# Performance work log

Hardware: AMD Instinct MI355X
Metric: run time of the kernel (lower is better)

The kernel has to match this reference:

```python
import jax, jax.numpy as jnp
from jax import lax
import numpy as np

G, K = 8, 9  # deformable groups, 3x3 kernel taps


def conv1x1_bn_relu(x, W, scale, bias):
    # Conv2d 1x1 (no bias) + folded eval-mode BatchNorm (per-channel scale/bias) + ReLU
    y = jnp.einsum('bchw,oc->bohw', x, W)
    return jax.nn.relu(y * scale[None, :, None, None] + bias[None, :, None, None])


def dcn_v2(feat, offset_feat, W_om, b_om, W_dcn, b_dcn):
    # Modulated deformable conv v2, 3x3, stride 1, pad 1, dilation 1,
    # deformable_groups=G, extra_offset_mask: offsets/mask predicted from offset_feat.
    B, C, H, W_ = feat.shape
    Cg = C // G
    om = lax.conv_general_dilated(offset_feat, W_om, (1, 1), ((1, 1), (1, 1)))
    om = om + b_om[None, :, None, None]              # [B, 3*G*K, H, W]
    o1, o2, m = jnp.split(om, 3, axis=1)
    off_y = o1.reshape(B, G, K, H, W_)
    off_x = o2.reshape(B, G, K, H, W_)
    mask = jax.nn.sigmoid(m).reshape(B, G, K, H, W_)
    dk = jnp.arange(3) - 1
    dkh = jnp.repeat(dk, 3)   # tap row offset,  k = kh*3 + kw
    dkw = jnp.tile(dk, 3)     # tap col offset
    hh = jnp.arange(H, dtype=feat.dtype)
    ww = jnp.arange(W_, dtype=feat.dtype)
    py = hh[None, None, None, :, None] + dkh[None, None, :, None, None].astype(feat.dtype) + off_y
    px = ww[None, None, None, None, :] + dkw[None, None, :, None, None].astype(feat.dtype) + off_x
    y0 = jnp.floor(py); x0 = jnp.floor(px)
    ty = py - y0; tx = px - x0
    xg = feat.reshape(B, G, Cg, H * W_)

    def gather(idx):  # idx [B,G,K,H,W] int32 -> [B,G,Cg,K,H,W]
        f = lambda xf, i: xf[:, i]
        return jax.vmap(jax.vmap(f))(xg, idx)

    val = jnp.zeros((B, G, Cg, K, H, W_), dtype=feat.dtype)
    y0i = y0.astype(jnp.int32); x0i = x0.astype(jnp.int32)
    for dy, wy in ((0, 1.0 - ty), (1, ty)):
        iy = y0i + dy
        vy = (iy >= 0) & (iy < H)
        iyc = jnp.clip(iy, 0, H - 1)
        for dx, wx in ((0, 1.0 - tx), (1, tx)):
            ix = x0i + dx
            v = vy & (ix >= 0) & (ix < W_)
            idx = iyc * W_ + jnp.clip(ix, 0, W_ - 1)
            w = (wy * wx) * v.astype(feat.dtype)      # zero-padding outside
            val = val + w[:, :, None] * gather(idx)
    val = val * mask[:, :, None]                      # modulation
    Wd = W_dcn.reshape(W_dcn.shape[0], G, Cg, K)      # [Cout, G, Cg, K]
    out = jnp.einsum('bgckhw,ogck->bohw', val, Wd) + b_dcn[None, :, None, None]
    return out


def setup_inputs() -> dict:
    key = jax.random.key(0)
    ks = jax.random.split(key, 16)
    B, C, H, W_ = 8, 128, 64, 64
    Cd = C // 2  # dcn out channels = 64
    d = {}
    d['feat_l'] = jax.random.normal(ks[0], (B, C, H, W_), jnp.float32)
    d['feat_s'] = jax.random.normal(ks[1], (B, C, H // 2, W_ // 2), jnp.float32)
    d['W_fsm'] = jax.random.normal(ks[2], (C, C), jnp.float32) / np.sqrt(C)
    d['s_fsm'] = 1.0 + 0.1 * jax.random.normal(ks[3], (C,), jnp.float32)
    d['b_fsm'] = 0.1 * jax.random.normal(ks[4], (C,), jnp.float32)
    d['W_off'] = jax.random.normal(ks[5], (C, 2 * C), jnp.float32) / np.sqrt(2 * C)
    d['s_off'] = 1.0 + 0.1 * jax.random.normal(ks[6], (C,), jnp.float32)
    d['b_off'] = 0.1 * jax.random.normal(ks[7], (C,), jnp.float32)
    d['W_om'] = 0.05 * jax.random.normal(ks[8], (3 * G * K, C, 3, 3), jnp.float32)
    d['b_om'] = jnp.zeros((3 * G * K,), jnp.float32)
    d['W_dcn'] = jax.random.normal(ks[9], (Cd, C, 3, 3), jnp.float32) / np.sqrt(C * 9)
    d['b_dcn'] = 0.1 * jax.random.normal(ks[10], (Cd,), jnp.float32)
    d['W_cat'] = jax.random.normal(ks[11], (C, Cd), jnp.float32) / np.sqrt(Cd)
    d['s_cat'] = 1.0 + 0.1 * jax.random.normal(ks[12], (C,), jnp.float32)
    d['b_cat'] = 0.1 * jax.random.normal(ks[13], (C,), jnp.float32)
    return d


def reference(feat_l, feat_s, W_fsm, s_fsm, b_fsm, W_off, s_off, b_off,
              W_om, b_om, W_dcn, b_dcn, W_cat, s_cat, b_cat):
    # nearest upsample x2 (F.interpolate nearest to feat_l spatial size)
    feat_up = jnp.repeat(jnp.repeat(feat_s, 2, axis=2), 2, axis=3)
    feat_arm = conv1x1_bn_relu(feat_l, W_fsm, s_fsm, b_fsm)
    offset = conv1x1_bn_relu(jnp.concatenate([feat_arm, feat_up * 2.0], axis=1),
                             W_off, s_off, b_off)
    feat_align = jax.nn.relu(dcn_v2(feat_up, offset, W_om, b_om, W_dcn, b_dcn))
    feat = conv1x1_bn_relu(feat_align, W_cat, s_cat, b_cat) + feat_arm
    return (feat, feat_arm)
```

## Files before the change

### kernel.cpp

```cpp
#include <hip/hip_runtime.h>


typedef __attribute__((ext_vector_type(8))) short short8;
typedef __attribute__((ext_vector_type(4))) float f32x4;
typedef _Float16 __attribute__((ext_vector_type(2))) h2;

static __device__ __forceinline__ unsigned short f2bf(float x) {
    union { float f; unsigned int u; } v; v.f = x;
    return (unsigned short)((v.u + 0x7FFF + ((v.u >> 16) & 1)) >> 16);
}
static __device__ __forceinline__ unsigned short f2h(float x) {
    union { _Float16 h; unsigned short u; } v; v.h = (_Float16)x;
    return v.u;
}

__global__ __launch_bounds__(256) void k_prep(const float* __restrict__ fs,
        uint4* __restrict__ fsT4, uint4* __restrict__ fsC4,
        const float* __restrict__ W_fsm, const float* __restrict__ W_off,
        const float* __restrict__ W_cat, const float* __restrict__ W_dcn,
        const float* __restrict__ W_om,
        unsigned short* __restrict__ wbfsm, unsigned short* __restrict__ wboff,
        unsigned short* __restrict__ wbcat, unsigned short* __restrict__ wbdcn,
        unsigned short* __restrict__ wb2) {
    __shared__ unsigned short st[64 * 136];
    const int t = threadIdx.x;
    if (blockIdx.x < 128) {
        unsigned int* st32 = (unsigned int*)st;
        const int b = blockIdx.x >> 4;
        const int p0 = (blockIdx.x & 15) << 6;
        for (int i = t; i < 64 * 64; i += 256) {
            int c2 = i >> 6, px = i & 63;
            float v0 = fs[(((b << 7) + 2 * c2) << 10) + p0 + px];
            float v1 = fs[(((b << 7) + 2 * c2 + 1) << 10) + p0 + px];
            st32[px * 68 + c2] = (unsigned int)f2bf(v0) | ((unsigned int)f2bf(v1) << 16);
        }
        __syncthreads();
        for (int i = t; i < 64 * 16; i += 256) {
            int px = i >> 4, q = i & 15;
            fsT4[(((b << 10) + p0 + px) << 4) + q] = ((const uint4*)(st + px * 136))[q];
        }
        __syncthreads();
        for (int i = t; i < 64 * 64; i += 256) {
            int c2 = i >> 6, px = i & 63;
            float v0 = fs[(((b << 7) + 2 * c2) << 10) + p0 + px];
            float v1 = fs[(((b << 7) + 2 * c2 + 1) << 10) + p0 + px];
            st32[px * 68 + c2] = (unsigned int)f2h(v0) | ((unsigned int)f2h(v1) << 16);
        }
        __syncthreads();
        for (int i = t; i < 64 * 16; i += 256) {
            int ci = i >> 6, px = i & 63;
            fsC4[(b << 14) + (ci << 10) + p0 + px] = ((const uint4*)(st + px * 136))[ci];
        }
        return;
    }
    int idx = (blockIdx.x - 128) * 256 + t;
    int lane = idx & 63;
    int ml = lane & 15, kl = (lane >> 4) * 8;
    unsigned short tmp[8];
    if (idx < 2048) {
        int r = idx >> 6;
        int o = (r % 8) * 16 + ml, k0 = (r / 8) * 32 + kl;
#pragma unroll
        for (int j = 0; j < 8; j++) tmp[j] = f2bf(W_fsm[o * 128 + k0 + j]);
        ((uint4*)wbfsm)[idx] = *(const uint4*)tmp;
    } else if (idx < 6144) {
        int i2 = idx - 2048;
        int r = i2 >> 6;
        int o = (r % 8) * 16 + ml, k0 = (r / 8) * 32 + kl;
#pragma unroll
        for (int j = 0; j < 8; j++) {
            int k = k0 + j;
            float f = W_off[o * 256 + k];
            if (k >= 128) f *= 2.0f;
            tmp[j] = f2bf(f);
        }
        ((uint4*)wboff)[i2] = *(const uint4*)tmp;
    } else if (idx < 7168) {
        int i2 = idx - 6144;
        int r = i2 >> 6;
        int o = (r % 8) * 16 + ml, k0 = (r / 8) * 32 + kl;
#pragma unroll
        for (int j = 0; j < 8; j++) tmp[j] = f2bf(W_cat[o * 64 + k0 + j]);
        ((uint4*)wbcat)[i2] = *(const uint4*)tmp;
    } else if (idx < 16384) {
        int i2 = idx - 7168;
        int r = i2 >> 6;
        int o = (r & 3) * 16 + ml, k0 = (r >> 2) * 32 + kl;
#pragma unroll
        for (int j = 0; j < 8; j++) {
            int k = k0 + j;
            int g = k / 144;
            int rem = k - g * 144;
            tmp[j] = f2h(W_dcn[(o * 128 + g * 16 + (rem & 15)) * 9 + (rem >> 4)]);
        }
        ((uint4*)wbdcn)[i2] = *(const uint4*)tmp;
    } else if (idx < 53248) {
        int i2 = idx - 16384;
        int r = i2 >> 6;
        int nt = r & 15, kk = r >> 4;
        int tap = kk >> 2, cc = kk & 3;
        int o = nt * 16 + ml;
        int c0 = cc * 32 + kl;
#pragma unroll
        for (int j = 0; j < 8; j++) {
            float v = (o < 216) ? W_om[(o * 128 + (c0 + j)) * 9 + tap] : 0.0f;
            tmp[j] = f2bf(v);
        }
        ((uint4*)wb2)[i2] = *(const uint4*)tmp;
    }
}

__global__ __launch_bounds__(512, 6) void k12(const float* __restrict__ feat_l,
        const uint4* __restrict__ fsT4,
        const unsigned short* __restrict__ wbf, const unsigned short* __restrict__ wbo,
        const float* __restrict__ s_fsm, const float* __restrict__ b_fsm,
        const float* __restrict__ s_off, const float* __restrict__ b_off,
        float* __restrict__ feat_arm, unsigned short* __restrict__ offT) {
    __shared__ unsigned short A1[64 * 136];
    __shared__ unsigned short A2[64 * 264];
    const int t = threadIdx.x;
    const int b = blockIdx.x >> 6;
    const int h = blockIdx.x & 63;
    const int hw0 = h << 6;
    unsigned int* A1w = (unsigned int*)A1;
    for (int i = t; i < 64 * 64; i += 512) {
        int c2 = i >> 6, px = i & 63;
        float v0 = feat_l[(((b << 7) + 2 * c2) << 12) + hw0 + px];
        float v1 = feat_l[(((b << 7) + 2 * c2 + 1) << 12) + hw0 + px];
        A1w[px * 68 + c2] = (unsigned int)f2bf(v0) | ((unsigned int)f2bf(v1) << 16);
    }
    {
        const int h2 = h >> 1;
        int px2 = t >> 4, q = t & 15;
        uint4 v = fsT4[(((b << 10) + (h2 << 5) + px2) << 4) + q];
        ((uint4*)(A2 + (2 * px2) * 264 + 128))[q] = v;
        ((uint4*)(A2 + (2 * px2 + 1) * 264 + 128))[q] = v;
    }
    __syncthreads();
    const int lane = t & 63;
    const int w = __builtin_amdgcn_readfirstlane(t >> 6);
    const int pq = w & 3;
    const int nh = w >> 2;
    const int m = lane & 15, ko = lane >> 4;
    f32x4 acc[4];
#pragma unroll
    for (int nt2 = 0; nt2 < 4; nt2++) acc[nt2] = (f32x4){0.f, 0.f, 0.f, 0.f};
#pragma unroll
    for (int kk = 0; kk < 4; kk++) {
        short8 av = *(const short8*)(A1 + (pq * 16 + m) * 136 + kk * 32 + ko * 8);
        const uint4* wb = (const uint4*)wbf + (kk * 8 + nh * 4) * 64 + lane;
#pragma unroll
        for (int nt2 = 0; nt2 < 4; nt2++) {
            uint4 bu = wb[nt2 * 64];
            acc[nt2] = __builtin_amdgcn_mfma_f32_16x16x32_bf16(av, *(short8*)&bu, acc[nt2], 0, 0, 0);
        }
    }
    {
        const int px0 = pq * 16 + (ko << 2);
#pragma unroll
        for (int nt2 = 0; nt2 < 4; nt2++) {
            int o = ((nh << 2) + nt2) * 16 + m;
            float sc = s_fsm[o], bi = b_fsm[o];
            f32x4 v;
#pragma unroll
            for (int r = 0; r < 4; r++) {
                float vv = fmaf(acc[nt2][r], sc, bi);
                vv = vv > 0.f ? vv : 0.f;
                v[r] = vv;
                A2[(px0 + r) * 264 + o] = f2bf(vv);
            }
            *(f32x4*)(feat_arm + ((((b << 7) + o) << 12) + hw0 + px0)) = v;
        }
    }
    __syncthreads();
    f32x4 acc2[4];
#pragma unroll
    for (int nt2 = 0; nt2 < 4; nt2++) acc2[nt2] = (f32x4){0.f, 0.f, 0.f, 0.f};
#pragma unroll
    for (int kk = 0; kk < 8; kk++) {
        short8 av = *(const short8*)(A2 + (pq * 16 + m) * 264 + kk * 32 + ko * 8);
        const uint4* wb = (const uint4*)wbo + (kk * 8 + nh * 4) * 64 + lane;
#pragma unroll
        for (int nt2 = 0; nt2 < 4; nt2++) {
            uint4 bu = wb[nt2 * 64];
            acc2[nt2] = __builtin_amdgcn_mfma_f32_16x16x32_bf16(av, *(short8*)&bu, acc2[nt2], 0, 0, 0);
        }
    }
    __syncthreads();
#pragma unroll
    for (int nt2 = 0; nt2 < 4; nt2++) {
        int o = ((nh << 2) + nt2) * 16 + m;
        float sc = s_off[o], bi = b_off[o];
#pragma unroll
        for (int r = 0; r < 4; r++) {
            float v = fmaf(acc2[nt2][r], sc, bi);
            v = v > 0.f ? v : 0.f;
            A2[(pq * 16 + ko * 4 + r) * 264 + o] = f2bf(v);
        }
    }
    __syncthreads();
    for (int i = t; i < 64 * 16; i += 512) {
        int px = i >> 4, q = i & 15;
        ((uint4*)offT)[(((b << 12) + hw0 + px) << 4) + q] = ((const uint4*)(A2 + px * 264))[q];
    }
}

static __device__ __forceinline__ void dcn_prep(int kk, int ko, const float* omrow,
        float fh, float fw, const uint4* __restrict__ fsC4, int b14,
        uint4& c00, uint4& c01, uint4& c10, uint4& c11,
        float& w00, float& w01, float& w10, float& w11) {
    int k0 = (kk << 5) + (ko << 3);
    int g = k0 / 144;
    int rem = k0 - g * 144;
    int tap = rem >> 4;
    int c0 = rem & 15;
    int ch = g * 9 + tap;
    float oy = omrow[ch];
    float ox = omrow[72 + ch];
    float mmv = omrow[144 + ch];
    mmv = 1.0f / (1.0f + __expf(-mmv));
    float py = fh + (float)(tap / 3 - 1) + oy;
    float pxx = fw + (float)(tap % 3 - 1) + ox;
    float y0f = floorf(py), x0f = floorf(pxx);
    float tyf = py - y0f, txf = pxx - x0f;
    int y0i = (int)y0f, x0i = (int)x0f;
    int y1i = y0i + 1, x1i = x0i + 1;
    bool vy0 = (y0i >= 0) && (y0i < 64);
    bool vy1 = (y1i >= 0) && (y1i < 64);
    bool vx0 = (x0i >= 0) && (x0i < 64);
    bool vx1 = (x1i >= 0) && (x1i < 64);
    w00 = (vy0 && vx0) ? (1.0f - tyf) * (1.0f - txf) * mmv : 0.0f;
    w01 = (vy0 && vx1) ? (1.0f - tyf) * txf * mmv : 0.0f;
    w10 = (vy1 && vx0) ? tyf * (1.0f - txf) * mmv : 0.0f;
    w11 = (vy1 && vx1) ? tyf * txf * mmv : 0.0f;
    int yc0 = y0i < 0 ? 0 : (y0i > 63 ? 63 : y0i);
    int yc1 = y1i < 0 ? 0 : (y1i > 63 ? 63 : y1i);
    int xc0 = x0i < 0 ? 0 : (x0i > 63 ? 63 : x0i);
    int xc1 = x1i < 0 ? 0 : (x1i > 63 ? 63 : x1i);
    int row0 = (yc0 >> 1) << 5, row1 = (yc1 >> 1) << 5;
    int ci = g * 2 + (c0 >> 3);
    const uint4* base = fsC4 + b14 + (ci << 10);
    c00 = base[row0 + (xc0 >> 1)];
    c01 = base[row0 + (xc1 >> 1)];
    c10 = base[row1 + (xc0 >> 1)];
    c11 = base[row1 + (xc1 >> 1)];
}

static __device__ __forceinline__ void dcn_consume(int kk,
        const uint4& c00, const uint4& c01, const uint4& c10, const uint4& c11,
        float w00, float w01, float w10, float w11,
        const uint4* __restrict__ wbd4, int lane, f32x4* accd) {
    _Float16 h00 = (_Float16)w00, h01 = (_Float16)w01;
    _Float16 h10 = (_Float16)w10, h11 = (_Float16)w11;
    h2 W00 = (h2){h00, h00}, W01 = (h2){h01, h01};
    h2 W10 = (h2){h10, h10}, W11 = (h2){h11, h11};
    union { uint4 u; h2 h[4]; } U00, U01, U10, U11;
    U00.u = c00; U01.u = c01; U10.u = c10; U11.u = c11;
    union { short8 s; h2 h[4]; } av;
#pragma unroll
    for (int c = 0; c < 4; c++)
        av.h[c] = U00.h[c] * W00 + U01.h[c] * W01 + U10.h[c] * W10 + U11.h[c] * W11;
    const uint4* wb = wbd4 + (kk << 2) * 64 + lane;
    __builtin_amdgcn_s_setprio(1);
#pragma unroll
    for (int nt = 0; nt < 4; nt++) {
        uint4 bu = wb[nt * 64];
        accd[nt] = __builtin_amdgcn_mfma_f32_16x16x32_f16(av.s, *(short8*)&bu, accd[nt], 0, 0, 0);
    }
    __builtin_amdgcn_s_setprio(0);
}

__global__ __launch_bounds__(512, 4) void k_omdcn(
        const unsigned short* __restrict__ offT, const uint4* __restrict__ fsC4,
        const unsigned short* __restrict__ Wb2, const float* __restrict__ bom,
        const unsigned short* __restrict__ wbd, const float* __restrict__ bd,
        const unsigned short* __restrict__ wbc,
        const float* __restrict__ s_cat, const float* __restrict__ b_cat,
        const float* __restrict__ feat_arm, float* __restrict__ feat) {
    __shared__ float LDSf[16384];
    unsigned short* st = (unsigned short*)LDSf;
    float* omT = LDSf;
    float* Rbuf = LDSf;
    unsigned short* A3 = (unsigned short*)(LDSf + 13888);
    const uint4* offT4 = (const uint4*)offT;
    const uint4* W4 = (const uint4*)Wb2;
    const uint4* wbd4 = (const uint4*)wbd;
    const int t = threadIdx.x;
    const int b = blockIdx.x >> 6;
    const int h = blockIdx.x & 63;
    for (int i = t; i < 3 * 66 * 16; i += 512) {
        int q = i & 15;
        int rp = i >> 4;
        int r = rp / 66, p = rp - r * 66;
        int gy = h + r - 1, gx = p - 1;
        uint4 v = make_uint4(0, 0, 0, 0);
        if (gy >= 0 && gy < 64 && gx >= 0 && gx < 64)
            v = offT4[((((b << 6) + gy) << 6) + gx) * 16 + q];
        ((uint4*)(st + rp * 136))[q] = v;
    }
    __syncthreads();
    const int lane = t & 63;
    const int w = __builtin_amdgcn_readfirstlane(t >> 6);
    const int m = lane & 15, ko = lane >> 4;
    f32x4 acc[2][4];
#pragma unroll
    for (int i = 0; i < 2; i++)
#pragma unroll
        for (int j = 0; j < 4; j++) acc[i][j] = (f32x4){0.f, 0.f, 0.f, 0.f};
    {
        const int ntb = w << 1;
        uint4 b4c[2];
#pragma unroll
        for (int nt2 = 0; nt2 < 2; nt2++)
            b4c[nt2] = W4[((ntb + nt2) << 6) + lane];
#pragma unroll
        for (int kk = 0; kk < 36; kk++) {
            const int tap = kk >> 2, cc = kk & 3;
            const int dy = tap / 3, dx = tap - dy * 3;
            uint4 b4n[2];
            if (kk < 35) {
#pragma unroll
                for (int nt2 = 0; nt2 < 2; nt2++)
                    b4n[nt2] = W4[((((kk + 1) << 4) + ntb + nt2) << 6) + lane];
            }
            short8 a8[4];
#pragma unroll
            for (int mt = 0; mt < 4; mt++) {
                int p = mt * 16 + m + dx;
                a8[mt] = *(const short8*)(st + (dy * 66 + p) * 136 + (cc << 5) + (ko << 3));
            }
            __builtin_amdgcn_s_setprio(1);
#pragma unroll
            for (int nt2 = 0; nt2 < 2; nt2++)
#pragma unroll
                for (int mt = 0; mt < 4; mt++)
                    acc[nt2][mt] = __builtin_amdgcn_mfma_f32_16x16x32_bf16(
                        a8[mt], *(short8*)&b4c[nt2], acc[nt2][mt], 0, 0, 0);
            __builtin_amdgcn_s_setprio(0);
            if (kk < 35) {
#pragma unroll
                for (int nt2 = 0; nt2 < 2; nt2++) b4c[nt2] = b4n[nt2];
            }
        }
    }
    __syncthreads();
#pragma unroll
    for (int nt2 = 0; nt2 < 2; nt2++) {
        int o = (((w << 1) + nt2) << 4) + m;
        if (o < 216) {
            float bv = bom[o];
#pragma unroll
            for (int mt = 0; mt < 4; mt++) {
                f32x4 v = acc[nt2][mt];
#pragma unroll
                for (int r = 0; r < 4; r++)
                    omT[(mt * 16 + (ko << 2) + r) * 217 + o] = v[r] + bv;
            }
        }
    }
    __syncthreads();
    const int nq = w & 3;
    const int kh = w >> 2;
    const int px = (nq << 4) + m;
    const float fh = (float)h, fw = (float)px;
    const int b14 = b << 14;
    const float* omrow = omT + px * 217;
    f32x4 accd[4];
#pragma unroll
    for (int nt = 0; nt < 4; nt++) accd[nt] = (f32x4){0.f, 0.f, 0.f, 0.f};
    {
        const int dk0 = kh * 18;
        uint4 s00[3], s01[3], s10[3], s11[3];
        float t00[3], t01[3], t10[3], t11[3];
#pragma unroll
        for (int i = 0; i < 2; i++)
            dcn_prep(dk0 + i, ko, omrow, fh, fw, fsC4, b14,
                     s00[i], s01[i], s10[i], s11[i], t00[i], t01[i], t10[i], t11[i]);
#pragma unroll
        for (int kki = 0; kki < 18; kki++) {
            const int sc_ = kki % 3;
            if (kki < 16) {
                const int sp = (kki + 2) % 3;
                dcn_prep(dk0 + kki + 2, ko, omrow, fh, fw, fsC4, b14,
                         s00[sp], s01[sp], s10[sp], s11[sp],
                         t00[sp], t01[sp], t10[sp], t11[sp]);
            }
            dcn_consume(dk0 + kki, s00[sc_], s01[sc_], s10[sc_], s11[sc_],
                        t00[sc_], t01[sc_], t10[sc_], t11[sc_], wbd4, lane, accd);
        }
    }
    __syncthreads();
    if (kh == 1) {
#pragma unroll
        for (int nt = 0; nt < 4; nt++)
            *(f32x4*)(Rbuf + ((nq << 6) + lane) * 20 + (nt << 2)) = accd[nt];
    }
    __syncthreads();
    if (kh == 0) {
#pragma unroll
        for (int nt = 0; nt < 4; nt++)
            accd[nt] += *(const f32x4*)(Rbuf + ((nq << 6) + lane) * 20 + (nt << 2));
#pragma unroll
        for (int nt = 0; nt < 4; nt++) {
            int o = (nt << 4) + m;
            float bv = bd[o];
#pragma unroll
            for (int r = 0; r < 4; r++) {
                float v = accd[nt][r] + bv;
                v = v > 0.f ? v : 0.f;
                A3[((nq << 4) + (ko << 2) + r) * 72 + o] = f2bf(v);
            }
        }
    }
    __syncthreads();
    f32x4 acc2[4];
#pragma unroll
    for (int nt2 = 0; nt2 < 4; nt2++) acc2[nt2] = (f32x4){0.f, 0.f, 0.f, 0.f};
#pragma unroll
    for (int kk2 = 0; kk2 < 2; kk2++) {
        short8 av = *(const short8*)(A3 + ((nq << 4) + m) * 72 + kk2 * 32 + (ko << 3));
#pragma unroll
        for (int nt2 = 0; nt2 < 4; nt2++) {
            uint4 bu = ((const uint4*)wbc)[(kk2 * 8 + (kh << 2) + nt2) * 64 + lane];
            acc2[nt2] = __builtin_amdgcn_mfma_f32_16x16x32_bf16(av, *(short8*)&bu, acc2[nt2], 0, 0, 0);
        }
    }
    {
        const int px0 = (nq << 4) + (ko << 2);
        const int base = (b << 19) + (h << 6) + px0;
        f32x4 fa[4];
#pragma unroll
        for (int nt2 = 0; nt2 < 4; nt2++) {
            int o = (((kh << 2) + nt2) << 4) + m;
            fa[nt2] = *(const f32x4*)(feat_arm + base + (o << 12));
        }
#pragma unroll
        for (int nt2 = 0; nt2 < 4; nt2++) {
            int o = (((kh << 2) + nt2) << 4) + m;
            float sc = s_cat[o], bi = b_cat[o];
            f32x4 v;
#pragma unroll
            for (int r = 0; r < 4; r++) {
                float vv = fmaf(acc2[nt2][r], sc, bi);
                vv = vv > 0.f ? vv : 0.f;
                v[r] = vv + fa[nt2][r];
            }
            *(f32x4*)(feat + base + (o << 12)) = v;
        }
    }
}

extern "C" void kernel_launch(void* const* d_in, const int* in_sizes, int n_in,
                              void* d_out, int out_size, void* d_ws, size_t ws_size,
                              hipStream_t stream) {
    const float* feat_l = (const float*)d_in[0];
    const float* feat_s = (const float*)d_in[1];
    const float* W_fsm  = (const float*)d_in[2];
    const float* s_fsm  = (const float*)d_in[3];
    const float* b_fsm  = (const float*)d_in[4];
    const float* W_off  = (const float*)d_in[5];
    const float* s_off  = (const float*)d_in[6];
    const float* b_off  = (const float*)d_in[7];
    const float* W_om   = (const float*)d_in[8];
    const float* b_om   = (const float*)d_in[9];
    const float* W_dcn  = (const float*)d_in[10];
    const float* b_dcn  = (const float*)d_in[11];
    const float* W_cat  = (const float*)d_in[12];
    const float* s_cat  = (const float*)d_in[13];
    const float* b_cat  = (const float*)d_in[14];

    float* feat     = (float*)d_out;
    float* feat_arm = feat + 4194304;

    float* ws = (float*)d_ws;
    unsigned short* offT = (unsigned short*)ws;
    uint4* fsT4  = (uint4*)(ws + 9175040);
    unsigned short* wb2   = (unsigned short*)(ws + 9699328);
    unsigned short* wbfsm = (unsigned short*)(ws + 9846784);
    unsigned short* wboff = (unsigned short*)(ws + 9854976);
    unsigned short* wbcat = (unsigned short*)(ws + 9871360);
    unsigned short* wbdcn = (unsigned short*)(ws + 9875456);
    uint4* fsC4  = (uint4*)(ws + 9912320);

    k_prep<<<336, 256, 0, stream>>>(feat_s, fsT4, fsC4, W_fsm, W_off, W_cat,
                                    W_dcn, W_om, wbfsm, wboff, wbcat, wbdcn, wb2);

    k12<<<512, 512, 0, stream>>>(feat_l, fsT4, wbfsm, wboff,
                                 s_fsm, b_fsm, s_off, b_off, feat_arm, offT);
    k_omdcn<<<512, 512, 0, stream>>>(offT, fsC4, wb2, b_om, wbdcn, b_dcn,
                                     wbcat, s_cat, b_cat, feat_arm, feat);
}
```

Measured before the change: 161.3 us.

## Retile MFMA wave work, trim padded offset-conv tiles, precompute sigmoid mask in LDS

Waves in the 1x1 conv GEMMs and the DCN stage now each compute a 2x2 block of MFMA tiles (two pixel tiles by two output tiles), so each A and B fragment load feeds two MFMAs. The offset/mask conv weight layout drops the padded 16th N tile (14 tiles instead of 16), and the eighth wave skips that GEMM. Offsets are split into separate y/x LDS arrays, and the mask sigmoid is applied once and stored as fp16, which shrinks LDS use. The DCN K-reduction is split four ways across waves with a two-level LDS reduction, which adds extra barriers.

```diff
diff --git a/kernel.cpp b/kernel.cpp
--- a/kernel.cpp
+++ b/kernel.cpp
@@ -94,10 +94,10 @@
             tmp[j] = f2h(W_dcn[(o * 128 + g * 16 + (rem & 15)) * 9 + (rem >> 4)]);
         }
         ((uint4*)wbdcn)[i2] = *(const uint4*)tmp;
-    } else if (idx < 53248) {
+    } else if (idx < 48640) {
         int i2 = idx - 16384;
         int r = i2 >> 6;
-        int nt = r & 15, kk = r >> 4;
+        int nt = r % 14, kk = r / 14;
         int tap = kk >> 2, cc = kk & 3;
         int o = nt * 16 + ml;
         int c0 = cc * 32 + kl;
@@ -139,32 +139,40 @@
     __syncthreads();
     const int lane = t & 63;
     const int w = __builtin_amdgcn_readfirstlane(t >> 6);
-    const int pq = w & 3;
-    const int nh = w >> 2;
+    const int ph = w & 1;
+    const int nq4 = w >> 1;
     const int m = lane & 15, ko = lane >> 4;
-    f32x4 acc[4];
-#pragma unroll
-    for (int nt2 = 0; nt2 < 4; nt2++) acc[nt2] = (f32x4){0.f, 0.f, 0.f, 0.f};
+    f32x4 acc[2][2];
+#pragma unroll
+    for (int i = 0; i < 2; i++)
+#pragma unroll
+        for (int j = 0; j < 2; j++) acc[i][j] = (f32x4){0.f, 0.f, 0.f, 0.f};
 #pragma unroll
     for (int kk = 0; kk < 4; kk++) {
-        short8 av = *(const short8*)(A1 + (pq * 16 + m) * 136 + kk * 32 + ko * 8);
-        const uint4* wb = (const uint4*)wbf + (kk * 8 + nh * 4) * 64 + lane;
-#pragma unroll
-        for (int nt2 = 0; nt2 < 4; nt2++) {
-            uint4 bu = wb[nt2 * 64];
-            acc[nt2] = __builtin_amdgcn_mfma_f32_16x16x32_bf16(av, *(short8*)&bu, acc[nt2], 0, 0, 0);
-        }
-    }
-    {
-        const int px0 = pq * 16 + (ko << 2);
-#pragma unroll
-        for (int nt2 = 0; nt2 < 4; nt2++) {
-            int o = ((nh << 2) + nt2) * 16 + m;
-            float sc = s_fsm[o], bi = b_fsm[o];
+        short8 a8[2];
+#pragma unroll
+        for (int mt = 0; mt < 2; mt++)
+            a8[mt] = *(const short8*)(A1 + ((ph << 5) + (mt << 4) + m) * 136 + kk * 32 + ko * 8);
+#pragma unroll
+        for (int nt2 = 0; nt2 < 2; nt2++) {
+            uint4 bu = ((const uint4*)wbf)[((kk << 3) + (nq4 << 1) + nt2) * 64 + lane];
+#pragma unroll
+            for (int mt = 0; mt < 2; mt++)
+                acc[mt][nt2] = __builtin_amdgcn_mfma_f32_16x16x32_bf16(
+                    a8[mt], *(short8*)&bu, acc[mt][nt2], 0, 0, 0);
+        }
+    }
+#pragma unroll
+    for (int nt2 = 0; nt2 < 2; nt2++) {
+        int o = (((nq4 << 1) + nt2) << 4) + m;
+        float sc = s_fsm[o], bi = b_fsm[o];
+#pragma unroll
+        for (int mt = 0; mt < 2; mt++) {
+            int px0 = (ph << 5) + (mt << 4) + (ko << 2);
             f32x4 v;
 #pragma unroll
             for (int r = 0; r < 4; r++) {
-                float vv = fmaf(acc[nt2][r], sc, bi);
+                float vv = fmaf(acc[mt][nt2][r], sc, bi);
                 vv = vv > 0.f ? vv : 0.f;
                 v[r] = vv;
                 A2[(px0 + r) * 264 + o] = f2bf(vv);
@@ -173,29 +181,40 @@
         }
     }
     __syncthreads();
-    f32x4 acc2[4];
-#pragma unroll
-    for (int nt2 = 0; nt2 < 4; nt2++) acc2[nt2] = (f32x4){0.f, 0.f, 0.f, 0.f};
+    f32x4 acc2[2][2];
+#pragma unroll
+    for (int i = 0; i < 2; i++)
+#pragma unroll
+        for (int j = 0; j < 2; j++) acc2[i][j] = (f32x4){0.f, 0.f, 0.f, 0.f};
 #pragma unroll
     for (int kk = 0; kk < 8; kk++) {
-        short8 av = *(const short8*)(A2 + (pq * 16 + m) * 264 + kk * 32 + ko * 8);
-        const uint4* wb = (const uint4*)wbo + (kk * 8 + nh * 4) * 64 + lane;
-#pragma unroll
-        for (int nt2 = 0; nt2 < 4; nt2++) {
-            uint4 bu = wb[nt2 * 64];
-            acc2[nt2] = __builtin_amdgcn_mfma_f32_16x16x32_bf16(av, *(short8*)&bu, acc2[nt2], 0, 0, 0);
-        }
-    }
-    __syncthreads();
-#pragma unroll
-    for (int nt2 = 0; nt2 < 4; nt2++) {
-        int o = ((nh << 2) + nt2) * 16 + m;
+        short8 a8[2];
+#pragma unroll
+        for (int mt = 0; mt < 2; mt++)
+            a8[mt] = *(const short8*)(A2 + ((ph << 5) + (mt << 4) + m) * 264 + kk * 32 + ko * 8);
+#pragma unroll
+        for (int nt2 = 0; nt2 < 2; nt2++) {
+            uint4 bu = ((const uint4*)wbo)[((kk << 3) + (nq4 << 1) + nt2) * 64 + lane];
+#pragma unroll
+            for (int mt = 0; mt < 2; mt++)
+                acc2[mt][nt2] = __builtin_amdgcn_mfma_f32_16x16x32_bf16(
+                    a8[mt], *(short8*)&bu, acc2[mt][nt2], 0, 0, 0);
+        }
+    }
+    __syncthreads();
+#pragma unroll
+    for (int nt2 = 0; nt2 < 2; nt2++) {
+        int o = (((nq4 << 1) + nt2) << 4) + m;
         float sc = s_off[o], bi = b_off[o];
 #pragma unroll
-        for (int r = 0; r < 4; r++) {
-            float v = fmaf(acc2[nt2][r], sc, bi);
-            v = v > 0.f ? v : 0.f;
-            A2[(pq * 16 + ko * 4 + r) * 264 + o] = f2bf(v);
+        for (int mt = 0; mt < 2; mt++) {
+            int px0 = (ph << 5) + (mt << 4) + (ko << 2);
+#pragma unroll
+            for (int r = 0; r < 4; r++) {
+                float v = fmaf(acc2[mt][nt2][r], sc, bi);
+                v = v > 0.f ? v : 0.f;
+                A2[(px0 + r) * 264 + o] = f2bf(v);
+            }
         }
     }
     __syncthreads();
@@ -205,8 +224,10 @@
     }
 }
 
-static __device__ __forceinline__ void dcn_prep(int kk, int ko, const float* omrow,
-        float fh, float fw, const uint4* __restrict__ fsC4, int b14,
+static __device__ __forceinline__ void dcn_prep(int kk, int ko,
+        const float* __restrict__ oyL, const float* __restrict__ oxL,
+        const unsigned short* __restrict__ mskL, int px,
+        float fh, const uint4* __restrict__ fsC4, int b14,
         uint4& c00, uint4& c01, uint4& c10, uint4& c11,
         float& w00, float& w01, float& w10, float& w11) {
     int k0 = (kk << 5) + (ko << 3);
@@ -215,12 +236,11 @@
     int tap = rem >> 4;
     int c0 = rem & 15;
     int ch = g * 9 + tap;
-    float oy = omrow[ch];
-    float ox = omrow[72 + ch];
-    float mmv = omrow[144 + ch];
-    mmv = 1.0f / (1.0f + __expf(-mmv));
+    float oy = oyL[px * 73 + ch];
+    float ox = oxL[px * 73 + ch];
+    float mmv = (float)(*(const _Float16*)(mskL + px * 74 + ch));
     float py = fh + (float)(tap / 3 - 1) + oy;
-    float pxx = fw + (float)(tap % 3 - 1) + ox;
+    float pxx = (float)px + (float)(tap % 3 - 1) + ox;
     float y0f = floorf(py), x0f = floorf(pxx);
     float tyf = py - y0f, txf = pxx - x0f;
     int y0i = (int)y0f, x0i = (int)x0f;
@@ -246,10 +266,10 @@
     c11 = base[row1 + (xc1 >> 1)];
 }
 
-static __device__ __forceinline__ void dcn_consume(int kk,
+static __device__ __forceinline__ void dcn_consume(
         const uint4& c00, const uint4& c01, const uint4& c10, const uint4& c11,
         float w00, float w01, float w10, float w11,
-        const uint4* __restrict__ wbd4, int lane, f32x4* accd) {
+        const uint4* __restrict__ wb, f32x4* accd) {
     _Float16 h00 = (_Float16)w00, h01 = (_Float16)w01;
     _Float16 h10 = (_Float16)w10, h11 = (_Float16)w11;
     h2 W00 = (h2){h00, h00}, W01 = (h2){h01, h01};
@@ -260,7 +280,6 @@
 #pragma unroll
     for (int c = 0; c < 4; c++)
         av.h[c] = U00.h[c] * W00 + U01.h[c] * W01 + U10.h[c] * W10 + U11.h[c] * W11;
-    const uint4* wb = wbd4 + (kk << 2) * 64 + lane;
     __builtin_amdgcn_s_setprio(1);
 #pragma unroll
     for (int nt = 0; nt < 4; nt++) {
@@ -277,11 +296,13 @@
         const unsigned short* __restrict__ wbc,
         const float* __restrict__ s_cat, const float* __restrict__ b_cat,
         const float* __restrict__ feat_arm, float* __restrict__ feat) {
-    __shared__ float LDSf[16384];
+    __shared__ float LDSf[13464];
     unsigned short* st = (unsigned short*)LDSf;
-    float* omT = LDSf;
+    float* oyL = LDSf;
+    float* oxL = LDSf + 4672;
+    unsigned short* mskL = (unsigned short*)(LDSf + 9344);
     float* Rbuf = LDSf;
-    unsigned short* A3 = (unsigned short*)(LDSf + 13888);
+    unsigned short* A3 = (unsigned short*)(LDSf + 9216);
     const uint4* offT4 = (const uint4*)offT;
     const uint4* W4 = (const uint4*)Wb2;
     const uint4* wbd4 = (const uint4*)wbd;
@@ -307,7 +328,7 @@
     for (int i = 0; i < 2; i++)
 #pragma unroll
         for (int j = 0; j < 4; j++) acc[i][j] = (f32x4){0.f, 0.f, 0.f, 0.f};
-    {
+    if (w < 7) {
         const int ntb = w << 1;
         uint4 b4c[2];
 #pragma unroll
@@ -321,7 +342,7 @@
             if (kk < 35) {
 #pragma unroll
                 for (int nt2 = 0; nt2 < 2; nt2++)
-                    b4n[nt2] = W4[((((kk + 1) << 4) + ntb + nt2) << 6) + lane];
+                    b4n[nt2] = W4[(((kk + 1) * 14 + ntb + nt2) << 6) + lane];
             }
             short8 a8[4];
 #pragma unroll
@@ -344,108 +365,148 @@
         }
     }
     __syncthreads();
-#pragma unroll
-    for (int nt2 = 0; nt2 < 2; nt2++) {
-        int o = (((w << 1) + nt2) << 4) + m;
-        if (o < 216) {
-            float bv = bom[o];
-#pragma unroll
-            for (int mt = 0; mt < 4; mt++) {
-                f32x4 v = acc[nt2][mt];
-#pragma unroll
-                for (int r = 0; r < 4; r++)
-                    omT[(mt * 16 + (ko << 2) + r) * 217 + o] = v[r] + bv;
-            }
-        }
-    }
-    __syncthreads();
-    const int nq = w & 3;
-    const int kh = w >> 2;
-    const int px = (nq << 4) + m;
-    const float fh = (float)h, fw = (float)px;
+    if (w < 7) {
+#pragma unroll
+        for (int nt2 = 0; nt2 < 2; nt2++) {
+            int o = (((w << 1) + nt2) << 4) + m;
+            if (o < 216) {
+                float bv = bom[o];
+#pragma unroll
+                for (int mt = 0; mt < 4; mt++) {
+                    f32x4 v = acc[nt2][mt];
+#pragma unroll
+                    for (int r = 0; r < 4; r++) {
+                        int px = mt * 16 + (ko << 2) + r;
+                        float val = v[r] + bv;
+                        if (o < 72) {
+                            oyL[px * 73 + o] = val;
+                        } else if (o < 144) {
+                            oxL[px * 73 + (o - 72)] = val;
+                        } else {
+                            float sg = 1.0f / (1.0f + __expf(-val));
+                            mskL[px * 74 + (o - 144)] = f2h(sg);
+                        }
+                    }
+                }
+            }
+        }
+    }
+    __syncthreads();
+    const int mh = w & 1;
+    const int kq = w >> 1;
+    const float fh = (float)h;
     const int b14 = b << 14;
-    const float* omrow = omT + px * 217;
-    f32x4 accd[4];
-#pragma unroll
-    for (int nt = 0; nt < 4; nt++) accd[nt] = (f32x4){0.f, 0.f, 0.f, 0.f};
+    f32x4 accd[2][4];
+#pragma unroll
+    for (int j = 0; j < 2; j++)
+#pragma unroll
+        for (int nt = 0; nt < 4; nt++) accd[j][nt] = (f32x4){0.f, 0.f, 0.f, 0.f};
     {
-        const int dk0 = kh * 18;
-        uint4 s00[3], s01[3], s10[3], s11[3];
-        float t00[3], t01[3], t10[3], t11[3];
-#pragma unroll
-        for (int i = 0; i < 2; i++)
-            dcn_prep(dk0 + i, ko, omrow, fh, fw, fsC4, b14,
-                     s00[i], s01[i], s10[i], s11[i], t00[i], t01[i], t10[i], t11[i]);
-#pragma unroll
-        for (int kki = 0; kki < 18; kki++) {
-            const int sc_ = kki % 3;
-            if (kki < 16) {
-                const int sp = (kki + 2) % 3;
-                dcn_prep(dk0 + kki + 2, ko, omrow, fh, fw, fsC4, b14,
-                         s00[sp], s01[sp], s10[sp], s11[sp],
-                         t00[sp], t01[sp], t10[sp], t11[sp]);
-            }
-            dcn_consume(dk0 + kki, s00[sc_], s01[sc_], s10[sc_], s11[sc_],
-                        t00[sc_], t01[sc_], t10[sc_], t11[sc_], wbd4, lane, accd);
-        }
-    }
-    __syncthreads();
-    if (kh == 1) {
-#pragma unroll
-        for (int nt = 0; nt < 4; nt++)
-            *(f32x4*)(Rbuf + ((nq << 6) + lane) * 20 + (nt << 2)) = accd[nt];
-    }
-    __syncthreads();
-    if (kh == 0) {
-#pragma unroll
-        for (int nt = 0; nt < 4; nt++)
-            accd[nt] += *(const f32x4*)(Rbuf + ((nq << 6) + lane) * 20 + (nt << 2));
+        const int dk0 = kq * 9;
+        const int px0 = (mh << 5) + m;
+#pragma unroll
+        for (int kki = 0; kki < 9; kki++) {
+            const int kk = dk0 + kki;
+            uint4 a00, a01, a10, a11, e00, e01, e10, e11;
+            float wa00, wa01, wa10, wa11, wb00, wb01, wb10, wb11;
+            dcn_prep(kk, ko, oyL, oxL, mskL, px0, fh, fsC4, b14,
+                     a00, a01, a10, a11, wa00, wa01, wa10, wa11);
+            dcn_prep(kk, ko, oyL, oxL, mskL, px0 + 16, fh, fsC4, b14,
+                     e00, e01, e10, e11, wb00, wb01, wb10, wb11);
+            const uint4* wb = wbd4 + (kk << 2) * 64 + lane;
+            dcn_consume(a00, a01, a10, a11, wa00, wa01, wa10, wa11, wb, accd[0]);
+            dcn_consume(e00, e01, e10, e11, wb00, wb01, wb10, wb11, wb, accd[1]);
+        }
+    }
+    __syncthreads();
+    if (kq >= 2) {
+        float* rb = Rbuf + ((((kq - 2) << 1) + mh) * 64 + lane) * 36;
+#pragma unroll
+        for (int j = 0; j < 2; j++)
+#pragma unroll
+            for (int nt = 0; nt < 4; nt++)
+                *(f32x4*)(rb + (j << 4) + (nt << 2)) = accd[j][nt];
+    }
+    __syncthreads();
+    if (kq < 2) {
+        const float* rb = Rbuf + (((kq << 1) + mh) * 64 + lane) * 36;
+#pragma unroll
+        for (int j = 0; j < 2; j++)
+#pragma unroll
+            for (int nt = 0; nt < 4; nt++)
+                accd[j][nt] += *(const f32x4*)(rb + (j << 4) + (nt << 2));
+    }
+    __syncthreads();
+    if (kq == 1) {
+        float* rb = Rbuf + (mh * 64 + lane) * 36;
+#pragma unroll
+        for (int j = 0; j < 2; j++)
+#pragma unroll
+            for (int nt = 0; nt < 4; nt++)
+                *(f32x4*)(rb + (j << 4) + (nt << 2)) = accd[j][nt];
+    }
+    __syncthreads();
+    if (kq == 0) {
+        const float* rb = Rbuf + (mh * 64 + lane) * 36;
+#pragma unroll
+        for (int j = 0; j < 2; j++)
+#pragma unroll
+            for (int nt = 0; nt < 4; nt++)
+                accd[j][nt] += *(const f32x4*)(rb + (j << 4) + (nt << 2));
 #pragma unroll
         for (int nt = 0; nt < 4; nt++) {
             int o = (nt << 4) + m;
             float bv = bd[o];
 #pragma unroll
-            for (int r = 0; r < 4; r++) {
-                float v = accd[nt][r] + bv;
-                v = v > 0.f ? v : 0.f;
-                A3[((nq << 4) + (ko << 2) + r) * 72 + o] = f2bf(v);
-            }
-        }
-    }
-    __syncthreads();
-    f32x4 acc2[4];
-#pragma unroll
-    for (int nt2 = 0; nt2 < 4; nt2++) acc2[nt2] = (f32x4){0.f, 0.f, 0.f, 0.f};
+            for (int j = 0; j < 2; j++)
+#pragma unroll
+                for (int r = 0; r < 4; r++) {
+                    float v = accd[j][nt][r] + bv;
+                    v = v > 0.f ? v : 0.f;
+                    A3[((mh << 5) + (j << 4) + (ko << 2) + r) * 72 + o] = f2bf(v);
+                }
+        }
+    }
+    __syncthreads();
+    f32x4 acc2[2][2];
+#pragma unroll
+    for (int i = 0; i < 2; i++)
+#pragma unroll
+        for (int j = 0; j < 2; j++) acc2[i][j] = (f32x4){0.f, 0.f, 0.f, 0.f};
 #pragma unroll
     for (int kk2 = 0; kk2 < 2; kk2++) {
-        short8 av = *(const short8*)(A3 + ((nq << 4) + m) * 72 + kk2 * 32 + (ko << 3));
-#pragma unroll
-        for (int nt2 = 0; nt2 < 4; nt2++) {
-            uint4 bu = ((const uint4*)wbc)[(kk2 * 8 + (kh << 2) + nt2) * 64 + lane];
-            acc2[nt2] = __builtin_amdgcn_mfma_f32_16x16x32_bf16(av, *(short8*)&bu, acc2[nt2], 0, 0, 0);
+        short8 a8[2];
+#pragma unroll
+        for (int mt = 0; mt < 2; mt++)
+            a8[mt] = *(const short8*)(A3 + ((mh << 5) + (mt << 4) + m) * 72 + kk2 * 32 + (ko << 3));
+#pragma unroll
+        for (int nt2 = 0; nt2 < 2; nt2++) {
+            uint4 bu = ((const uint4*)wbc)[((kk2 << 3) + (kq << 1) + nt2) * 64 + lane];
+#pragma unroll
+            for (int mt = 0; mt < 2; mt++)
+                acc2[mt][nt2] = __builtin_amdgcn_mfma_f32_16x16x32_bf16(
+                    a8[mt], *(short8*)&bu, acc2[mt][nt2], 0, 0, 0);
         }
     }
     {
-        const int px0 = (nq << 4) + (ko << 2);
-        const int base = (b << 19) + (h << 6) + px0;
-        f32x4 fa[4];
-#pragma unroll
-        for (int nt2 = 0; nt2 < 4; nt2++) {
-            int o = (((kh << 2) + nt2) << 4) + m;
-            fa[nt2] = *(const f32x4*)(feat_arm + base + (o << 12));
-        }
-#pragma unroll
-        for (int nt2 = 0; nt2 < 4; nt2++) {
-            int o = (((kh << 2) + nt2) << 4) + m;
+#pragma unroll
+        for (int nt2 = 0; nt2 < 2; nt2++) {
+            int o = (((kq << 1) + nt2) << 4) + m;
             float sc = s_cat[o], bi = b_cat[o];
-            f32x4 v;
-#pragma unroll
-            for (int r = 0; r < 4; r++) {
-                float vv = fmaf(acc2[nt2][r], sc, bi);
-                vv = vv > 0.f ? vv : 0.f;
-                v[r] = vv + fa[nt2][r];
-            }
-            *(f32x4*)(feat + base + (o << 12)) = v;
+#pragma unroll
+            for (int mt = 0; mt < 2; mt++) {
+                int px0 = (mh << 5) + (mt << 4) + (ko << 2);
+                int gidx = (b << 19) + (o << 12) + (h << 6) + px0;
+                f32x4 fa = *(const f32x4*)(feat_arm + gidx);
+                f32x4 v;
+#pragma unroll
+                for (int r = 0; r < 4; r++) {
+                    float vv = fmaf(acc2[mt][nt2][r], sc, bi);
+                    vv = vv > 0.f ? vv : 0.f;
+                    v[r] = vv + fa[r];
+                }
+                *(f32x4*)(feat + gidx) = v;
+            }
         }
     }
 }
@@ -482,7 +543,7 @@
     unsigned short* wbdcn = (unsigned short*)(ws + 9875456);
     uint4* fsC4  = (uint4*)(ws + 9912320);
 
-    k_prep<<<336, 256, 0, stream>>>(feat_s, fsT4, fsC4, W_fsm, W_off, W_cat,
+    k_prep<<<318, 256, 0, stream>>>(feat_s, fsT4, fsC4, W_fsm, W_off, W_cat,
                                     W_dcn, W_om, wbfsm, wboff, wbcat, wbdcn, wb2);
 
     k12<<<512, 512, 0, stream>>>(feat_l, fsT4, wbfsm, wboff,
```

Measured after the change: 159.0 us. No clear change (-1.4%).

## Trim offset-conv padding tiles, retile k12 MFMA, hoist mask sigmoid

Applied to the files above, without the earlier changes.

The offset/mask conv weights are now packed into 14 N-tiles instead of 16, so the padded all-zero tiles beyond output channel 216 are no longer computed and wave 7 skips the MFMA loop. The mask sigmoid moves from the per-sample DCN prep into the om epilogue, so it runs once per value rather than once per use. k12's 1x1 conv waves are retiled from 16x64 to 32x32 output blocks, which reuses A fragments across two M tiles and halves the B loads per wave. One wave sits idle during the om conv, which adds some imbalance.

```diff
diff --git a/kernel.cpp b/kernel.cpp
--- a/kernel.cpp
+++ b/kernel.cpp
@@ -94,10 +94,10 @@
             tmp[j] = f2h(W_dcn[(o * 128 + g * 16 + (rem & 15)) * 9 + (rem >> 4)]);
         }
         ((uint4*)wbdcn)[i2] = *(const uint4*)tmp;
-    } else if (idx < 53248) {
+    } else if (idx < 48640) {
         int i2 = idx - 16384;
         int r = i2 >> 6;
-        int nt = r & 15, kk = r >> 4;
+        int nt = r % 14, kk = r / 14;
         int tap = kk >> 2, cc = kk & 3;
         int o = nt * 16 + ml;
         int c0 = cc * 32 + kl;
@@ -139,32 +139,40 @@
     __syncthreads();
     const int lane = t & 63;
     const int w = __builtin_amdgcn_readfirstlane(t >> 6);
-    const int pq = w & 3;
-    const int nh = w >> 2;
+    const int ph = w & 1;
+    const int nq4 = w >> 1;
     const int m = lane & 15, ko = lane >> 4;
-    f32x4 acc[4];
-#pragma unroll
-    for (int nt2 = 0; nt2 < 4; nt2++) acc[nt2] = (f32x4){0.f, 0.f, 0.f, 0.f};
+    f32x4 acc[2][2];
+#pragma unroll
+    for (int i = 0; i < 2; i++)
+#pragma unroll
+        for (int j = 0; j < 2; j++) acc[i][j] = (f32x4){0.f, 0.f, 0.f, 0.f};
 #pragma unroll
     for (int kk = 0; kk < 4; kk++) {
-        short8 av = *(const short8*)(A1 + (pq * 16 + m) * 136 + kk * 32 + ko * 8);
-        const uint4* wb = (const uint4*)wbf + (kk * 8 + nh * 4) * 64 + lane;
-#pragma unroll
-        for (int nt2 = 0; nt2 < 4; nt2++) {
-            uint4 bu = wb[nt2 * 64];
-            acc[nt2] = __builtin_amdgcn_mfma_f32_16x16x32_bf16(av, *(short8*)&bu, acc[nt2], 0, 0, 0);
-        }
-    }
-    {
-        const int px0 = pq * 16 + (ko << 2);
-#pragma unroll
-        for (int nt2 = 0; nt2 < 4; nt2++) {
-            int o = ((nh << 2) + nt2) * 16 + m;
-            float sc = s_fsm[o], bi = b_fsm[o];
+        short8 a8[2];
+#pragma unroll
+        for (int mt = 0; mt < 2; mt++)
+            a8[mt] = *(const short8*)(A1 + ((ph << 5) + (mt << 4) + m) * 136 + kk * 32 + ko * 8);
+#pragma unroll
+        for (int nt2 = 0; nt2 < 2; nt2++) {
+            uint4 bu = ((const uint4*)wbf)[((kk << 3) + (nq4 << 1) + nt2) * 64 + lane];
+#pragma unroll
+            for (int mt = 0; mt < 2; mt++)
+                acc[mt][nt2] = __builtin_amdgcn_mfma_f32_16x16x32_bf16(
+                    a8[mt], *(short8*)&bu, acc[mt][nt2], 0, 0, 0);
+        }
+    }
+#pragma unroll
+    for (int nt2 = 0; nt2 < 2; nt2++) {
+        int o = (((nq4 << 1) + nt2) << 4) + m;
+        float sc = s_fsm[o], bi = b_fsm[o];
+#pragma unroll
+        for (int mt = 0; mt < 2; mt++) {
+            int px0 = (ph << 5) + (mt << 4) + (ko << 2);
             f32x4 v;
 #pragma unroll
             for (int r = 0; r < 4; r++) {
-                float vv = fmaf(acc[nt2][r], sc, bi);
+                float vv = fmaf(acc[mt][nt2][r], sc, bi);
                 vv = vv > 0.f ? vv : 0.f;
                 v[r] = vv;
                 A2[(px0 + r) * 264 + o] = f2bf(vv);
@@ -173,29 +181,40 @@
         }
     }
     __syncthreads();
-    f32x4 acc2[4];
-#pragma unroll
-    for (int nt2 = 0; nt2 < 4; nt2++) acc2[nt2] = (f32x4){0.f, 0.f, 0.f, 0.f};
+    f32x4 acc2[2][2];
+#pragma unroll
+    for (int i = 0; i < 2; i++)
+#pragma unroll
+        for (int j = 0; j < 2; j++) acc2[i][j] = (f32x4){0.f, 0.f, 0.f, 0.f};
 #pragma unroll
     for (int kk = 0; kk < 8; kk++) {
-        short8 av = *(const short8*)(A2 + (pq * 16 + m) * 264 + kk * 32 + ko * 8);
-        const uint4* wb = (const uint4*)wbo + (kk * 8 + nh * 4) * 64 + lane;
-#pragma unroll
-        for (int nt2 = 0; nt2 < 4; nt2++) {
-            uint4 bu = wb[nt2 * 64];
-            acc2[nt2] = __builtin_amdgcn_mfma_f32_16x16x32_bf16(av, *(short8*)&bu, acc2[nt2], 0, 0, 0);
-        }
-    }
-    __syncthreads();
-#pragma unroll
-    for (int nt2 = 0; nt2 < 4; nt2++) {
-        int o = ((nh << 2) + nt2) * 16 + m;
+        short8 a8[2];
+#pragma unroll
+        for (int mt = 0; mt < 2; mt++)
+            a8[mt] = *(const short8*)(A2 + ((ph << 5) + (mt << 4) + m) * 264 + kk * 32 + ko * 8);
+#pragma unroll
+        for (int nt2 = 0; nt2 < 2; nt2++) {
+            uint4 bu = ((const uint4*)wbo)[((kk << 3) + (nq4 << 1) + nt2) * 64 + lane];
+#pragma unroll
+            for (int mt = 0; mt < 2; mt++)
+                acc2[mt][nt2] = __builtin_amdgcn_mfma_f32_16x16x32_bf16(
+                    a8[mt], *(short8*)&bu, acc2[mt][nt2], 0, 0, 0);
+        }
+    }
+    __syncthreads();
+#pragma unroll
+    for (int nt2 = 0; nt2 < 2; nt2++) {
+        int o = (((nq4 << 1) + nt2) << 4) + m;
         float sc = s_off[o], bi = b_off[o];
 #pragma unroll
-        for (int r = 0; r < 4; r++) {
-            float v = fmaf(acc2[nt2][r], sc, bi);
-            v = v > 0.f ? v : 0.f;
-            A2[(pq * 16 + ko * 4 + r) * 264 + o] = f2bf(v);
+        for (int mt = 0; mt < 2; mt++) {
+            int px0 = (ph << 5) + (mt << 4) + (ko << 2);
+#pragma unroll
+            for (int r = 0; r < 4; r++) {
+                float v = fmaf(acc2[mt][nt2][r], sc, bi);
+                v = v > 0.f ? v : 0.f;
+                A2[(px0 + r) * 264 + o] = f2bf(v);
+            }
         }
     }
     __syncthreads();
@@ -218,7 +237,6 @@
     float oy = omrow[ch];
     float ox = omrow[72 + ch];
     float mmv = omrow[144 + ch];
-    mmv = 1.0f / (1.0f + __expf(-mmv));
     float py = fh + (float)(tap / 3 - 1) + oy;
     float pxx = fw + (float)(tap % 3 - 1) + ox;
     float y0f = floorf(py), x0f = floorf(pxx);
@@ -307,7 +325,7 @@
     for (int i = 0; i < 2; i++)
 #pragma unroll
         for (int j = 0; j < 4; j++) acc[i][j] = (f32x4){0.f, 0.f, 0.f, 0.f};
-    {
+    if (w < 7) {
         const int ntb = w << 1;
         uint4 b4c[2];
 #pragma unroll
@@ -321,7 +339,7 @@
             if (kk < 35) {
 #pragma unroll
                 for (int nt2 = 0; nt2 < 2; nt2++)
-                    b4n[nt2] = W4[((((kk + 1) << 4) + ntb + nt2) << 6) + lane];
+                    b4n[nt2] = W4[(((kk + 1) * 14 + ntb + nt2) << 6) + lane];
             }
             short8 a8[4];
 #pragma unroll
@@ -344,17 +362,23 @@
         }
     }
     __syncthreads();
-#pragma unroll
-    for (int nt2 = 0; nt2 < 2; nt2++) {
-        int o = (((w << 1) + nt2) << 4) + m;
-        if (o < 216) {
-            float bv = bom[o];
-#pragma unroll
-            for (int mt = 0; mt < 4; mt++) {
-                f32x4 v = acc[nt2][mt];
-#pragma unroll
-                for (int r = 0; r < 4; r++)
-                    omT[(mt * 16 + (ko << 2) + r) * 217 + o] = v[r] + bv;
+    if (w < 7) {
+#pragma unroll
+        for (int nt2 = 0; nt2 < 2; nt2++) {
+            int o = (((w << 1) + nt2) << 4) + m;
+            if (o < 216) {
+                float bv = bom[o];
+                bool ismask = (o >= 144);
+#pragma unroll
+                for (int mt = 0; mt < 4; mt++) {
+                    f32x4 v = acc[nt2][mt];
+#pragma unroll
+                    for (int r = 0; r < 4; r++) {
+                        float val = v[r] + bv;
+                        if (ismask) val = 1.0f / (1.0f + __expf(-val));
+                        omT[(mt * 16 + (ko << 2) + r) * 217 + o] = val;
+                    }
+                }
             }
         }
     }
@@ -482,7 +506,7 @@
     unsigned short* wbdcn = (unsigned short*)(ws + 9875456);
     uint4* fsC4  = (uint4*)(ws + 9912320);
 
-    k_prep<<<336, 256, 0, stream>>>(feat_s, fsT4, fsC4, W_fsm, W_off, W_cat,
+    k_prep<<<318, 256, 0, stream>>>(feat_s, fsT4, fsC4, W_fsm, W_off, W_cat,
                                     W_dcn, W_om, wbfsm, wboff, wbcat, wbdcn, wb2);
 
     k12<<<512, 512, 0, stream>>>(feat_l, fsT4, wbfsm, wboff,
```

Result: faster. 158.1 us (-2.0%).
